# Kernel optimization log

Hardware: AMD Instinct MI355X
Metric: run time of the kernel (lower is better)

## Reference

```python
import jax, jax.numpy as jnp
import numpy as np

B, L, D = 16, 512, 128   # batch of sequences, seq len, input_dim
BN_EPS = 1e-5
TEMP = 1.0


def setup_inputs() -> dict:
    key = jax.random.key(0)
    ks = jax.random.split(key, 5)
    ids = jax.random.randint(ks[0], (B, L), 0, 50000)            # item ids per (seq, pos)
    log_mask = jnp.ones((B, L), dtype=jnp.int32)                 # all positions valid (static N)
    x1 = jax.random.normal(ks[1], (B * L, D), dtype=jnp.float32)
    x2 = jax.random.normal(ks[2], (B * L, D), dtype=jnp.float32)
    w1 = jax.random.normal(ks[3], (2 * D, D), dtype=jnp.float32) * 0.05  # torch Linear: [out, in]
    b1 = jnp.zeros((2 * D,), jnp.float32)
    w2 = jax.random.normal(ks[4], (D, 2 * D), dtype=jnp.float32) * 0.05
    b2 = jnp.zeros((D,), jnp.float32)
    gamma = jnp.ones((D,), jnp.float32)   # BatchNorm1d affine weight
    beta = jnp.zeros((D,), jnp.float32)   # BatchNorm1d affine bias
    return dict(ids=ids, log_mask=log_mask, x1=x1, x2=x2,
                w1=w1, b1=b1, w2=w2, b2=b2, gamma=gamma, beta=beta)


def _embed(x, w1, b1, w2, b2, gamma, beta):
    """linear1 -> relu -> linear2 -> BatchNorm1d (train-mode batch stats) -> L2 normalize."""
    h = jax.nn.relu(x @ w1.T + b1)
    y = h @ w2.T + b2
    mu = y.mean(axis=0)
    var = ((y - mu) ** 2).mean(axis=0)          # biased var, as torch BN uses for normalization
    y = (y - mu) * jax.lax.rsqrt(var + BN_EPS) * gamma + beta
    return y / jnp.linalg.norm(y, axis=1, keepdims=True)


def reference(ids, log_mask, x1, x2, w1, b1, w2, b2, gamma, beta):
    # log_mask is all-nonzero in this setup, so the gather by nonzero indices is the identity.
    nb, nl = ids.shape
    N = x1.shape[0]                      # = nb * nl valid anchors
    ids_f = ids.reshape(-1)
    seq = jnp.repeat(jnp.arange(nb), nl)  # seq_indexs: which sequence each row belongs to

    z1 = _embed(x1, w1, b1, w2, b2, gamma, beta)
    z2 = _embed(x2, w1, b1, w2, b2, gamma, beta)
    S = z1 @ z2.T                        # [N, N] cosine similarity (rows already unit-norm)

    idx = jnp.arange(N)
    ids_next = jnp.roll(ids_f, -1)
    seq_next = jnp.roll(seq, -1)
    # two-positive branch: i < N-1 and same sequence as the next row
    two = (idx < N - 1) & (seq == seq_next)            # [N] bool

    diag = jnp.diagonal(S)                             # cos(anchor_i, input2_i)
    s_next = S[idx, (idx + 1) % N]                     # cos(anchor_i, input2_{i+1})

    cols = idx[None, :]
    neg1 = ids_f[None, :] != ids_f[:, None]                                # single-pos negatives
    neg2 = neg1 & (ids_f[None, :] != ids_next[:, None]) & (seq[None, :] != seq[:, None])
    mask = jnp.where(two[:, None], neg2, neg1)
    # add the positives (self, and i+1 in the two-positive branch)
    mask = mask | (cols == idx[:, None]) | (two[:, None] & (cols == idx[:, None] + 1))

    denom = jnp.sum(jnp.where(mask, jnp.exp(S / TEMP), 0.0), axis=1)       # [N]
    pos_sum = diag + jnp.where(two, s_next, 0.0)
    n_pos = 1.0 + two.astype(S.dtype)

    inner = -(pos_sum / TEMP - jnp.log(denom)) / n_pos
    return jnp.sum(inner) / N
```

## Files before the change

### kernel.cpp

```cpp
#include <hip/hip_runtime.h>

#define N_TOT 8192
#define SEQ_L 512
#define D 128
#define NCHUNK 16
#define CHUNK (N_TOT / NCHUNK)
#define NJT (CHUNK / 64)
#define LOG2E 1.4426950408889634f
#define LN2   0.6931471805599453f

using bf16x8  = __attribute__((ext_vector_type(8))) short;
using f32x4   = __attribute__((ext_vector_type(4))) float;

static __device__ __forceinline__ unsigned short f2bf(float f) {
    unsigned int u = __float_as_uint(f);
    u = (u + 0x7FFFu + ((u >> 16) & 1u)) >> 16;
    return (unsigned short)u;
}
static __device__ __forceinline__ float bf2f(unsigned short h) {
    return __uint_as_float(((unsigned int)h) << 16);
}
static __device__ __forceinline__ float dot8(bf16x8 a, bf16x8 b) {
    float s = 0.f;
    #pragma unroll
    for (int k = 0; k < 8; ++k)
        s = fmaf(bf2f((unsigned short)a[k]), bf2f((unsigned short)b[k]), s);
    return s;
}

__global__ __launch_bounds__(256) void convert_w_kernel(
    const float* __restrict__ w1, const float* __restrict__ w2,
    unsigned short* __restrict__ w1b, unsigned short* __restrict__ w2b)
{
    int idx = blockIdx.x * 256 + threadIdx.x;
    const float* src = (idx < 8192) ? w1 : w2;
    unsigned short* dst = (idx < 8192) ? w1b : w2b;
    int off = ((idx < 8192) ? idx : idx - 8192) * 4;
    float4 v = *(const float4*)(src + off);
    ushort4 o;
    o.x = f2bf(v.x); o.y = f2bf(v.y); o.z = f2bf(v.z); o.w = f2bf(v.w);
    *(ushort4*)(dst + off) = o;
}

__global__ __launch_bounds__(256) void mlp_mfma_kernel(
    const float* __restrict__ x1, const float* __restrict__ x2,
    const unsigned short* __restrict__ w1b, const float* __restrict__ b1,
    const unsigned short* __restrict__ w2b, const float* __restrict__ b2,
    unsigned short* __restrict__ z1, unsigned short* __restrict__ z2,
    float* __restrict__ part_s, float* __restrict__ part_ss)
{
    __shared__ unsigned short hsh[32][264];
    const int t = threadIdx.x;
    const int w = t >> 6;
    const int lane = t & 63;
    const int g = lane >> 4;
    const int c16 = lane & 15;
    const int tensor = blockIdx.x >> 8;
    const int blk = blockIdx.x & 255;
    const int r0 = blk * 32;
    const float* __restrict__ x = tensor ? x2 : x1;
    unsigned short* __restrict__ z = tensor ? z2 : z1;

    bf16x8 af[2][4];
    #pragma unroll
    for (int rf = 0; rf < 2; ++rf)
        #pragma unroll
        for (int ks = 0; ks < 4; ++ks) {
            const float* xp = x + (size_t)(r0 + rf * 16 + c16) * D + ks * 32 + g * 8;
            float4 u0 = *(const float4*)xp;
            float4 u1 = *(const float4*)(xp + 4);
            bf16x8 a;
            a[0] = f2bf(u0.x); a[1] = f2bf(u0.y); a[2] = f2bf(u0.z); a[3] = f2bf(u0.w);
            a[4] = f2bf(u1.x); a[5] = f2bf(u1.y); a[6] = f2bf(u1.z); a[7] = f2bf(u1.w);
            af[rf][ks] = a;
        }
    f32x4 acc1[2][4] = {};
    #pragma unroll
    for (int ks = 0; ks < 4; ++ks)
        #pragma unroll
        for (int nf = 0; nf < 4; ++nf) {
            int n = w * 64 + nf * 16 + c16;
            bf16x8 b = *(const bf16x8*)(w1b + (size_t)n * D + ks * 32 + g * 8);
            #pragma unroll
            for (int rf = 0; rf < 2; ++rf)
                acc1[rf][nf] = __builtin_amdgcn_mfma_f32_16x16x32_bf16(af[rf][ks], b, acc1[rf][nf], 0, 0, 0);
        }
    #pragma unroll
    for (int nf = 0; nf < 4; ++nf) {
        float bb = b1[w * 64 + nf * 16 + c16];
        #pragma unroll
        for (int rf = 0; rf < 2; ++rf)
            #pragma unroll
            for (int r = 0; r < 4; ++r)
                hsh[rf * 16 + g * 4 + r][w * 64 + nf * 16 + c16] = f2bf(fmaxf(acc1[rf][nf][r] + bb, 0.f));
    }
    __syncthreads();

    f32x4 acc2[2][2] = {};
    #pragma unroll
    for (int ks = 0; ks < 8; ++ks) {
        bf16x8 a0 = *(const bf16x8*)(&hsh[c16][ks * 32 + g * 8]);
        bf16x8 a1 = *(const bf16x8*)(&hsh[16 + c16][ks * 32 + g * 8]);
        #pragma unroll
        for (int nf = 0; nf < 2; ++nf) {
            int n = w * 32 + nf * 16 + c16;
            bf16x8 b = *(const bf16x8*)(w2b + (size_t)n * 256 + ks * 32 + g * 8);
            acc2[0][nf] = __builtin_amdgcn_mfma_f32_16x16x32_bf16(a0, b, acc2[0][nf], 0, 0, 0);
            acc2[1][nf] = __builtin_amdgcn_mfma_f32_16x16x32_bf16(a1, b, acc2[1][nf], 0, 0, 0);
        }
    }

    #pragma unroll
    for (int nf = 0; nf < 2; ++nf) {
        int col = w * 32 + nf * 16 + c16;
        float bb = b2[col];
        float s = 0.f, ss = 0.f;
        #pragma unroll
        for (int rf = 0; rf < 2; ++rf)
            #pragma unroll
            for (int r = 0; r < 4; ++r) {
                float v = acc2[rf][nf][r] + bb;
                z[(size_t)(r0 + rf * 16 + g * 4 + r) * D + col] = f2bf(v);
                s += v; ss += v * v;
            }
        s  += __shfl_xor(s, 16);  s  += __shfl_xor(s, 32);
        ss += __shfl_xor(ss, 16); ss += __shfl_xor(ss, 32);
        if (g == 0) {
            part_s [((size_t)tensor * 256 + blk) * D + col] = s;
            part_ss[((size_t)tensor * 256 + blk) * D + col] = ss;
        }
    }
}

__global__ __launch_bounds__(256) void bn_reduce_kernel(
    const float* __restrict__ part_s, const float* __restrict__ part_ss,
    const float* __restrict__ gamma,
    float* __restrict__ mu, float* __restrict__ sc)
{
    const int t = threadIdx.x;
    const int tensor = blockIdx.x >> 7;
    const int col = blockIdx.x & 127;
    float s  = part_s [((size_t)tensor * 256 + t) * D + col];
    float ss = part_ss[((size_t)tensor * 256 + t) * D + col];
    #pragma unroll
    for (int m = 32; m; m >>= 1) { s += __shfl_xor(s, m); ss += __shfl_xor(ss, m); }
    __shared__ float rs[4], rss[4];
    if ((t & 63) == 0) { rs[t >> 6] = s; rss[t >> 6] = ss; }
    __syncthreads();
    if (t == 0) {
        float S = rs[0] + rs[1] + rs[2] + rs[3];
        float SS = rss[0] + rss[1] + rss[2] + rss[3];
        float m = S / (float)N_TOT;
        float var = SS / (float)N_TOT - m * m;
        mu[tensor * D + col] = m;
        sc[tensor * D + col] = gamma[col] * rsqrtf(var + 1e-5f);
    }
}

__global__ __launch_bounds__(256) void bn_l2_kernel(
    unsigned short* __restrict__ z1, unsigned short* __restrict__ z2,
    const float* __restrict__ mu, const float* __restrict__ sc,
    const float* __restrict__ beta)
{
    const int t = threadIdx.x;
    const int tensor = blockIdx.x >> 11;
    const int row = (blockIdx.x & 2047) * 4 + (t >> 6);
    const int lane = t & 63;
    unsigned short* __restrict__ yr = (tensor ? z2 : z1) + (size_t)row * D;
    const float* __restrict__ mub = mu + tensor * D;
    const float* __restrict__ scb = sc + tensor * D;

    ushort2 v = ((const ushort2*)yr)[lane];
    float2 m2 = ((const float2*)mub)[lane];
    float2 s2 = ((const float2*)scb)[lane];
    float2 b2 = ((const float2*)beta)[lane];
    float v0 = (bf2f(v.x) - m2.x) * s2.x + b2.x;
    float v1 = (bf2f(v.y) - m2.y) * s2.y + b2.y;
    float ssq = v0 * v0 + v1 * v1;
    #pragma unroll
    for (int m = 32; m; m >>= 1) ssq += __shfl_xor(ssq, m);
    float rn = rsqrtf(ssq);
    if (tensor == 0) rn *= LOG2E;
    ushort2 o; o.x = f2bf(v0 * rn); o.y = f2bf(v1 * rn);
    ((ushort2*)yr)[lane] = o;
}

__global__ __launch_bounds__(256) void diag_kernel(
    const short* __restrict__ z1, const short* __restrict__ z2,
    const int* __restrict__ ids,
    float* __restrict__ posv, float* __restrict__ dden)
{
    const int t = threadIdx.x;
    if (blockIdx.x < 256) {
        const int row = blockIdx.x * 32 + (t >> 3);
        const int le = t & 7;
        const short* ap = z1 + (size_t)row * D + le * 16;
        const short* bp = z2 + (size_t)row * D + le * 16;
        const short* cp = z2 + (size_t)((row + 1) & (N_TOT - 1)) * D + le * 16;
        bf16x8 a0 = *(const bf16x8*)ap, a1 = *(const bf16x8*)(ap + 8);
        float s1 = dot8(a0, *(const bf16x8*)bp) + dot8(a1, *(const bf16x8*)(bp + 8));
        float s2 = dot8(a0, *(const bf16x8*)cp) + dot8(a1, *(const bf16x8*)(cp + 8));
        #pragma unroll
        for (int m = 1; m < 8; m <<= 1) { s1 += __shfl_xor(s1, m); s2 += __shfl_xor(s2, m); }
        if (le == 0) {
            bool two = (row & (SEQ_L - 1)) != (SEQ_L - 1);
            if (two) {
                posv[row] = (s1 + s2) * LN2;
                dden[row] = exp2f(s1) + exp2f(s2);
            } else {
                posv[row] = s1 * LN2;
            }
        }
    } else {
        const int sr = blockIdx.x - 256;
        const int i = sr * SEQ_L + (SEQ_L - 1);
        const int jbase = sr * SEQ_L;
        const int idi_ = ids[i];
        float acc = 0.f;
        #pragma unroll
        for (int c = 0; c < 2; ++c) {
            int j = jbase + t * 2 + c;
            float s = 0.f;
            for (int k = 0; k < 16; ++k) {
                bf16x8 va = *(const bf16x8*)(z1 + (size_t)i * D + k * 8);
                bf16x8 vb = *(const bf16x8*)(z2 + (size_t)j * D + k * 8);
                s += dot8(va, vb);
            }
            bool m = (ids[j] != idi_) | (j == i);
            acc += m ? exp2f(s) : 0.f;
        }
        #pragma unroll
        for (int m = 32; m; m >>= 1) acc += __shfl_xor(acc, m);
        __shared__ float red[4];
        if ((t & 63) == 0) red[t >> 6] = acc;
        __syncthreads();
        if (t == 0) dden[i] = red[0] + red[1] + red[2] + red[3];
    }
}

__global__ __launch_bounds__(256) void loss_mfma_kernel(
    const short* __restrict__ z1, const short* __restrict__ z2,
    const int* __restrict__ ids,
    float* __restrict__ den_part)
{
    const int t    = threadIdx.x;
    const int w    = t >> 6;
    const int lane = t & 63;
    const int g    = lane >> 4;
    const int c16  = lane & 15;

    const int c15 = blockIdx.x >> 6;
    const int rbi = blockIdx.x & 63;
    const int rb  = rbi * 128;
    const int seqb = rbi >> 2;
    const int chunk = c15 + (c15 >= seqb);
    const int jbase = chunk * CHUNK;

    const int i_wb = rb + w * 32;

    __shared__ __align__(16) unsigned char z2s[2][64 * 256];

    const int srow = t >> 2;
    const int sq   = t & 3;

    bf16x8 af[2][4];
    #pragma unroll
    for (int rf = 0; rf < 2; ++rf)
        #pragma unroll
        for (int ks = 0; ks < 4; ++ks)
            af[rf][ks] = *(const bf16x8*)(z1 + (size_t)(i_wb + rf * 16 + c16) * D + ks * 32 + g * 8);

    int idi[2][4], idn_s[2][4];
    #pragma unroll
    for (int rf = 0; rf < 2; ++rf)
        #pragma unroll
        for (int r = 0; r < 4; ++r) {
            int i = i_wb + rf * 16 + g * 4 + r;
            idi[rf][r] = ids[i];
            bool tw = ((i & (SEQ_L - 1)) != (SEQ_L - 1));
            idn_s[rf][r] = tw ? ids[(i + 1) & (N_TOT - 1)] : idi[rf][r];
        }

    #pragma unroll
    for (int it = 0; it < 4; ++it) {
        bf16x8 v = *(const bf16x8*)(z2 + (size_t)(jbase + srow) * D + sq * 8 + it * 32);
        int byte = (sq * 16 + it * 64) ^ ((srow & 7) << 4);
        *(bf16x8*)&z2s[0][srow * 256 + byte] = v;
    }
    int idj[4];
    #pragma unroll
    for (int nf = 0; nf < 4; ++nf) idj[nf] = ids[jbase + nf * 16 + c16];
    __syncthreads();

    float den_acc[2][4] = {};
    int cbuf = 0;

    #pragma unroll 1
    for (int jt = 0; jt < NJT; ++jt) {
        const int cb = jbase + jt * 64;

        bf16x8 stg[4];
        int idjn[4];
        if (jt + 1 < NJT) {
            #pragma unroll
            for (int it = 0; it < 4; ++it)
                stg[it] = *(const bf16x8*)(z2 + (size_t)(cb + 64 + srow) * D + sq * 8 + it * 32);
            #pragma unroll
            for (int nf = 0; nf < 4; ++nf) idjn[nf] = ids[cb + 64 + nf * 16 + c16];
        }

        f32x4 acc[2][4] = {};
        #pragma unroll
        for (int ks = 0; ks < 4; ++ks)
            #pragma unroll
            for (int nf = 0; nf < 4; ++nf) {
                int r = nf * 16 + c16;
                int byte = (ks * 64 + g * 16) ^ ((r & 7) << 4);
                bf16x8 b = *(const bf16x8*)&z2s[cbuf][r * 256 + byte];
                acc[0][nf] = __builtin_amdgcn_mfma_f32_16x16x32_bf16(af[0][ks], b, acc[0][nf], 0, 0, 0);
                acc[1][nf] = __builtin_amdgcn_mfma_f32_16x16x32_bf16(af[1][ks], b, acc[1][nf], 0, 0, 0);
            }

        #pragma unroll
        for (int rf = 0; rf < 2; ++rf)
            #pragma unroll
            for (int nf = 0; nf < 4; ++nf)
                #pragma unroll
                for (int r = 0; r < 4; ++r) {
                    float e = exp2f(acc[rf][nf][r]);
                    bool m = (idj[nf] != idi[rf][r]) & (idj[nf] != idn_s[rf][r]);
                    den_acc[rf][r] += m ? e : 0.f;
                }

        if (jt + 1 < NJT) {
            #pragma unroll
            for (int it = 0; it < 4; ++it) {
                int byte = (sq * 16 + it * 64) ^ ((srow & 7) << 4);
                *(bf16x8*)&z2s[cbuf ^ 1][srow * 256 + byte] = stg[it];
            }
            #pragma unroll
            for (int nf = 0; nf < 4; ++nf) idj[nf] = idjn[nf];
        }
        __syncthreads();
        cbuf ^= 1;
    }

    #pragma unroll
    for (int rf = 0; rf < 2; ++rf)
        #pragma unroll
        for (int r = 0; r < 4; ++r) {
            float dsum = den_acc[rf][r];
            #pragma unroll
            for (int m = 8; m; m >>= 1) dsum += __shfl_xor(dsum, m);
            if (c16 == 0)
                den_part[chunk * N_TOT + i_wb + rf * 16 + g * 4 + r] = dsum;
        }
}

__global__ __launch_bounds__(1024) void loss_finish_kernel(
    const float* __restrict__ den_part, const float* __restrict__ posv,
    const float* __restrict__ dden, float* __restrict__ out)
{
    const int t = threadIdx.x;
    float v = 0.f;
    for (int k = 0; k < N_TOT / 1024; ++k) {
        int row = t + k * 1024;
        int seqb = row >> 9;
        float den = dden[row];
        #pragma unroll
        for (int q = 0; q < NCHUNK; ++q)
            if (q != seqb) den += den_part[q * N_TOT + row];
        bool two = ((row & (SEQ_L - 1)) != (SEQ_L - 1));
        float npos = two ? 2.f : 1.f;
        v += -(posv[row] - logf(den)) / npos;
    }
    #pragma unroll
    for (int m = 32; m; m >>= 1) v += __shfl_xor(v, m);
    __shared__ float red[16];
    if ((t & 63) == 0) red[t >> 6] = v;
    __syncthreads();
    if (t == 0) {
        float tot = 0.f;
        #pragma unroll
        for (int i = 0; i < 16; ++i) tot += red[i];
        out[0] = tot / (float)N_TOT;
    }
}

extern "C" void kernel_launch(void* const* d_in, const int* in_sizes, int n_in,
                              void* d_out, int out_size, void* d_ws, size_t ws_size,
                              hipStream_t stream)
{
    const int*   ids   = (const int*)d_in[0];
    const float* x1    = (const float*)d_in[2];
    const float* x2    = (const float*)d_in[3];
    const float* w1    = (const float*)d_in[4];
    const float* b1    = (const float*)d_in[5];
    const float* w2    = (const float*)d_in[6];
    const float* b2    = (const float*)d_in[7];
    const float* gamma = (const float*)d_in[8];
    const float* beta  = (const float*)d_in[9];

    char* ws = (char*)d_ws;
    unsigned short* z1b = (unsigned short*)ws;
    unsigned short* z2b = (unsigned short*)(ws + (2u << 20));
    float* part_s  = (float*)(ws + (4u << 20));
    float* part_ss = part_s + 2 * 256 * D;
    float* mu      = part_ss + 2 * 256 * D;
    float* sc      = mu + 2 * D;
    float* den_part = sc + 2 * D;
    float* posv    = den_part + NCHUNK * N_TOT;
    float* dden    = posv + N_TOT;
    unsigned short* w1b = (unsigned short*)(dden + N_TOT);
    unsigned short* w2b = w1b + 256 * D;

    convert_w_kernel<<<64, 256, 0, stream>>>(w1, w2, w1b, w2b);
    mlp_mfma_kernel<<<512, 256, 0, stream>>>(x1, x2, w1b, b1, w2b, b2,
                                             z1b, z2b, part_s, part_ss);
    bn_reduce_kernel<<<256, 256, 0, stream>>>(part_s, part_ss, gamma, mu, sc);
    bn_l2_kernel<<<4096, 256, 0, stream>>>(z1b, z2b, mu, sc, beta);
    diag_kernel<<<272, 256, 0, stream>>>((const short*)z1b, (const short*)z2b,
                                         ids, posv, dden);
    loss_mfma_kernel<<<960, 256, 0, stream>>>((const short*)z1b, (const short*)z2b,
                                              ids, den_part);
    loss_finish_kernel<<<1, 1024, 0, stream>>>(den_part, posv, dden, (float*)d_out);
}
```

Before: 89.45 us.

## Remove id masking from cross-sequence loss tile; subtract rare id collisions separately

The cross-sequence MFMA tile loop no longer loads ids or evaluates the negative mask per element. It sums exp over all columns, and a new corr_kernel computes the exp of the rare masked-out entries (id matches with the anchor or next id) so the finish kernel can subtract them. The loop is also restructured: the last tile is peeled, the LDS store and barrier move before the exp accumulation, and the kernel gets an occupancy hint in its launch bounds. The trade-off is an extra kernel that scans all ids for every row, plus possible cancellation error from subtracting large exp terms.

```diff
diff --git a/kernel.cpp b/kernel.cpp
--- a/kernel.cpp
+++ b/kernel.cpp
@@ -238,9 +238,58 @@
     }
 }
 
-__global__ __launch_bounds__(256) void loss_mfma_kernel(
+__global__ __launch_bounds__(256) void corr_kernel(
     const short* __restrict__ z1, const short* __restrict__ z2,
-    const int* __restrict__ ids,
+    const int* __restrict__ ids, float* __restrict__ corr)
+{
+    const int t = threadIdx.x;
+    const int w = t >> 6;
+    const int lane = t & 63;
+    const int rbase = blockIdx.x * 8 + w * 2;
+
+    int   idi[2], idn[2], seqi[2];
+    bool  two[2];
+    float cr[2] = {0.f, 0.f};
+    #pragma unroll
+    for (int rr = 0; rr < 2; ++rr) {
+        int i = rbase + rr;
+        idi[rr] = ids[i];
+        idn[rr] = ids[(i + 1) & (N_TOT - 1)];
+        two[rr] = (i & (SEQ_L - 1)) != (SEQ_L - 1);
+        seqi[rr] = i >> 9;
+    }
+
+    for (int k = 0; k < N_TOT / 64; ++k) {
+        int j = lane + k * 64;
+        int idj = ids[j];
+        int seqj = j >> 9;
+        #pragma unroll
+        for (int rr = 0; rr < 2; ++rr) {
+            bool hit = (seqj != seqi[rr]) &&
+                       ((idj == idi[rr]) || (two[rr] && idj == idn[rr]));
+            if (hit) {
+                int i = rbase + rr;
+                float s = 0.f;
+                for (int k2 = 0; k2 < 16; ++k2) {
+                    bf16x8 va = *(const bf16x8*)(z1 + (size_t)i * D + k2 * 8);
+                    bf16x8 vb = *(const bf16x8*)(z2 + (size_t)j * D + k2 * 8);
+                    s += dot8(va, vb);
+                }
+                cr[rr] += exp2f(s);
+            }
+        }
+    }
+    #pragma unroll
+    for (int rr = 0; rr < 2; ++rr) {
+        float v = cr[rr];
+        #pragma unroll
+        for (int m = 32; m; m >>= 1) v += __shfl_xor(v, m);
+        if (lane == 0) corr[rbase + rr] = v;
+    }
+}
+
+__global__ __launch_bounds__(256, 4) void loss_mfma_kernel(
+    const short* __restrict__ z1, const short* __restrict__ z2,
     float* __restrict__ den_part)
 {
     const int t    = threadIdx.x;
@@ -262,6 +311,8 @@
 
     const int srow = t >> 2;
     const int sq   = t & 3;
+    const int wxor = (srow & 7) << 4;
+    const int rxor = (c16 & 7) << 4;
 
     bf16x8 af[2][4];
     #pragma unroll
@@ -270,79 +321,67 @@
         for (int ks = 0; ks < 4; ++ks)
             af[rf][ks] = *(const bf16x8*)(z1 + (size_t)(i_wb + rf * 16 + c16) * D + ks * 32 + g * 8);
 
-    int idi[2][4], idn_s[2][4];
-    #pragma unroll
-    for (int rf = 0; rf < 2; ++rf)
-        #pragma unroll
-        for (int r = 0; r < 4; ++r) {
-            int i = i_wb + rf * 16 + g * 4 + r;
-            idi[rf][r] = ids[i];
-            bool tw = ((i & (SEQ_L - 1)) != (SEQ_L - 1));
-            idn_s[rf][r] = tw ? ids[(i + 1) & (N_TOT - 1)] : idi[rf][r];
-        }
-
     #pragma unroll
     for (int it = 0; it < 4; ++it) {
         bf16x8 v = *(const bf16x8*)(z2 + (size_t)(jbase + srow) * D + sq * 8 + it * 32);
-        int byte = (sq * 16 + it * 64) ^ ((srow & 7) << 4);
-        *(bf16x8*)&z2s[0][srow * 256 + byte] = v;
-    }
-    int idj[4];
-    #pragma unroll
-    for (int nf = 0; nf < 4; ++nf) idj[nf] = ids[jbase + nf * 16 + c16];
+        *(bf16x8*)&z2s[0][srow * 256 + ((sq * 16 + it * 64) ^ wxor)] = v;
+    }
     __syncthreads();
 
     float den_acc[2][4] = {};
     int cbuf = 0;
 
     #pragma unroll 1
-    for (int jt = 0; jt < NJT; ++jt) {
+    for (int jt = 0; jt < NJT - 1; ++jt) {
         const int cb = jbase + jt * 64;
 
         bf16x8 stg[4];
-        int idjn[4];
-        if (jt + 1 < NJT) {
-            #pragma unroll
-            for (int it = 0; it < 4; ++it)
-                stg[it] = *(const bf16x8*)(z2 + (size_t)(cb + 64 + srow) * D + sq * 8 + it * 32);
-            #pragma unroll
-            for (int nf = 0; nf < 4; ++nf) idjn[nf] = ids[cb + 64 + nf * 16 + c16];
-        }
+        #pragma unroll
+        for (int it = 0; it < 4; ++it)
+            stg[it] = *(const bf16x8*)(z2 + (size_t)(cb + 64 + srow) * D + sq * 8 + it * 32);
 
         f32x4 acc[2][4] = {};
         #pragma unroll
         for (int ks = 0; ks < 4; ++ks)
             #pragma unroll
             for (int nf = 0; nf < 4; ++nf) {
-                int r = nf * 16 + c16;
-                int byte = (ks * 64 + g * 16) ^ ((r & 7) << 4);
-                bf16x8 b = *(const bf16x8*)&z2s[cbuf][r * 256 + byte];
+                bf16x8 b = *(const bf16x8*)&z2s[cbuf][(nf * 16 + c16) * 256 + ((ks * 64 + g * 16) ^ rxor)];
                 acc[0][nf] = __builtin_amdgcn_mfma_f32_16x16x32_bf16(af[0][ks], b, acc[0][nf], 0, 0, 0);
                 acc[1][nf] = __builtin_amdgcn_mfma_f32_16x16x32_bf16(af[1][ks], b, acc[1][nf], 0, 0, 0);
             }
 
         #pragma unroll
+        for (int it = 0; it < 4; ++it)
+            *(bf16x8*)&z2s[cbuf ^ 1][srow * 256 + ((sq * 16 + it * 64) ^ wxor)] = stg[it];
+        __syncthreads();
+
+        #pragma unroll
         for (int rf = 0; rf < 2; ++rf)
             #pragma unroll
             for (int nf = 0; nf < 4; ++nf)
                 #pragma unroll
-                for (int r = 0; r < 4; ++r) {
-                    float e = exp2f(acc[rf][nf][r]);
-                    bool m = (idj[nf] != idi[rf][r]) & (idj[nf] != idn_s[rf][r]);
-                    den_acc[rf][r] += m ? e : 0.f;
-                }
-
-        if (jt + 1 < NJT) {
-            #pragma unroll
-            for (int it = 0; it < 4; ++it) {
-                int byte = (sq * 16 + it * 64) ^ ((srow & 7) << 4);
-                *(bf16x8*)&z2s[cbuf ^ 1][srow * 256 + byte] = stg[it];
-            }
-            #pragma unroll
-            for (int nf = 0; nf < 4; ++nf) idj[nf] = idjn[nf];
-        }
-        __syncthreads();
+                for (int r = 0; r < 4; ++r)
+                    den_acc[rf][r] += exp2f(acc[rf][nf][r]);
         cbuf ^= 1;
+    }
+
+    {
+        f32x4 acc[2][4] = {};
+        #pragma unroll
+        for (int ks = 0; ks < 4; ++ks)
+            #pragma unroll
+            for (int nf = 0; nf < 4; ++nf) {
+                bf16x8 b = *(const bf16x8*)&z2s[cbuf][(nf * 16 + c16) * 256 + ((ks * 64 + g * 16) ^ rxor)];
+                acc[0][nf] = __builtin_amdgcn_mfma_f32_16x16x32_bf16(af[0][ks], b, acc[0][nf], 0, 0, 0);
+                acc[1][nf] = __builtin_amdgcn_mfma_f32_16x16x32_bf16(af[1][ks], b, acc[1][nf], 0, 0, 0);
+            }
+        #pragma unroll
+        for (int rf = 0; rf < 2; ++rf)
+            #pragma unroll
+            for (int nf = 0; nf < 4; ++nf)
+                #pragma unroll
+                for (int r = 0; r < 4; ++r)
+                    den_acc[rf][r] += exp2f(acc[rf][nf][r]);
     }
 
     #pragma unroll
@@ -359,14 +398,15 @@
 
 __global__ __launch_bounds__(1024) void loss_finish_kernel(
     const float* __restrict__ den_part, const float* __restrict__ posv,
-    const float* __restrict__ dden, float* __restrict__ out)
+    const float* __restrict__ dden, const float* __restrict__ corr,
+    float* __restrict__ out)
 {
     const int t = threadIdx.x;
     float v = 0.f;
     for (int k = 0; k < N_TOT / 1024; ++k) {
         int row = t + k * 1024;
         int seqb = row >> 9;
-        float den = dden[row];
+        float den = dden[row] - corr[row];
         #pragma unroll
         for (int q = 0; q < NCHUNK; ++q)
             if (q != seqb) den += den_part[q * N_TOT + row];
@@ -411,7 +451,8 @@
     float* den_part = sc + 2 * D;
     float* posv    = den_part + NCHUNK * N_TOT;
     float* dden    = posv + N_TOT;
-    unsigned short* w1b = (unsigned short*)(dden + N_TOT);
+    float* corr    = dden + N_TOT;
+    unsigned short* w1b = (unsigned short*)(corr + N_TOT);
     unsigned short* w2b = w1b + 256 * D;
 
     convert_w_kernel<<<64, 256, 0, stream>>>(w1, w2, w1b, w2b);
@@ -421,7 +462,10 @@
     bn_l2_kernel<<<4096, 256, 0, stream>>>(z1b, z2b, mu, sc, beta);
     diag_kernel<<<272, 256, 0, stream>>>((const short*)z1b, (const short*)z2b,
                                          ids, posv, dden);
+    corr_kernel<<<1024, 256, 0, stream>>>((const short*)z1b, (const short*)z2b,
+                                          ids, corr);
     loss_mfma_kernel<<<960, 256, 0, stream>>>((const short*)z1b, (const short*)z2b,
-                                              ids, den_part);
-    loss_finish_kernel<<<1, 1024, 0, stream>>>(den_part, posv, dden, (float*)d_out);
-}
+                                              den_part);
+    loss_finish_kernel<<<1, 1024, 0, stream>>>(den_part, posv, dden, corr,
+                                               (float*)d_out);
+}
```

After: 114.9 us. 1.28x slower.

## Compute unmasked full-row exp sums and subtract sparse id-match corrections

Applied to the files above, without the earlier changes.

The dense loss kernel now sums exp(S) over every column without id masks. It computes all 16 chunks, including the own-sequence chunk, and drops the LDS staging in favour of direct per-wave global loads of z2 fragments. A new corr_kernel scans the ids per row and subtracts the exp terms of the rare columns whose id matches. The finish kernel swaps the own-sequence chunk for the diagonal term on two-positive rows. This removes per-element mask compares and the special-cased chunk skipping, at the cost of computing 1/16 more of the matrix, a serial per-row id scan, and loss of LDS reuse of z2 across waves.

```diff
diff --git a/kernel.cpp b/kernel.cpp
--- a/kernel.cpp
+++ b/kernel.cpp
@@ -5,7 +5,6 @@
 #define D 128
 #define NCHUNK 16
 #define CHUNK (N_TOT / NCHUNK)
-#define NJT (CHUNK / 64)
 #define LOG2E 1.4426950408889634f
 #define LN2   0.6931471805599453f
 
@@ -187,60 +186,79 @@
 
 __global__ __launch_bounds__(256) void diag_kernel(
     const short* __restrict__ z1, const short* __restrict__ z2,
-    const int* __restrict__ ids,
     float* __restrict__ posv, float* __restrict__ dden)
 {
     const int t = threadIdx.x;
-    if (blockIdx.x < 256) {
-        const int row = blockIdx.x * 32 + (t >> 3);
-        const int le = t & 7;
-        const short* ap = z1 + (size_t)row * D + le * 16;
-        const short* bp = z2 + (size_t)row * D + le * 16;
-        const short* cp = z2 + (size_t)((row + 1) & (N_TOT - 1)) * D + le * 16;
-        bf16x8 a0 = *(const bf16x8*)ap, a1 = *(const bf16x8*)(ap + 8);
-        float s1 = dot8(a0, *(const bf16x8*)bp) + dot8(a1, *(const bf16x8*)(bp + 8));
-        float s2 = dot8(a0, *(const bf16x8*)cp) + dot8(a1, *(const bf16x8*)(cp + 8));
-        #pragma unroll
-        for (int m = 1; m < 8; m <<= 1) { s1 += __shfl_xor(s1, m); s2 += __shfl_xor(s2, m); }
-        if (le == 0) {
-            bool two = (row & (SEQ_L - 1)) != (SEQ_L - 1);
-            if (two) {
-                posv[row] = (s1 + s2) * LN2;
-                dden[row] = exp2f(s1) + exp2f(s2);
-            } else {
-                posv[row] = s1 * LN2;
+    const int row = blockIdx.x * 32 + (t >> 3);
+    const int le = t & 7;
+    const short* ap = z1 + (size_t)row * D + le * 16;
+    const short* bp = z2 + (size_t)row * D + le * 16;
+    const short* cp = z2 + (size_t)((row + 1) & (N_TOT - 1)) * D + le * 16;
+    bf16x8 a0 = *(const bf16x8*)ap, a1 = *(const bf16x8*)(ap + 8);
+    float s1 = dot8(a0, *(const bf16x8*)bp) + dot8(a1, *(const bf16x8*)(bp + 8));
+    float s2 = dot8(a0, *(const bf16x8*)cp) + dot8(a1, *(const bf16x8*)(cp + 8));
+    #pragma unroll
+    for (int m = 1; m < 8; m <<= 1) { s1 += __shfl_xor(s1, m); s2 += __shfl_xor(s2, m); }
+    if (le == 0) {
+        bool two = (row & (SEQ_L - 1)) != (SEQ_L - 1);
+        if (two) {
+            posv[row] = (s1 + s2) * LN2;
+            dden[row] = exp2f(s1) + exp2f(s2);
+        } else {
+            posv[row] = s1 * LN2;
+        }
+    }
+}
+
+__global__ __launch_bounds__(256) void corr_kernel(
+    const short* __restrict__ z1, const short* __restrict__ z2,
+    const int* __restrict__ ids, float* __restrict__ corr)
+{
+    const int t = threadIdx.x;
+    const int row = blockIdx.x * 32 + (t >> 3);
+    const int le = t & 7;
+
+    const bool two = (row & (SEQ_L - 1)) != (SEQ_L - 1);
+    const int idi  = ids[row];
+    const int idn_s = two ? ids[(row + 1) & (N_TOT - 1)] : idi;
+    const int seq_s = two ? (row >> 9) : -1;
+
+    float cr = 0.f;
+    const int4* idv = (const int4*)ids;
+    #pragma unroll 4
+    for (int k = 0; k < 256; ++k) {
+        int jb = le * 256 + k;
+        int4 v = idv[jb];
+        int j0 = jb * 4;
+        if ((j0 >> 9) != seq_s) {
+            int hm = (((v.x == idi) | (v.x == idn_s)) & (j0 + 0 != row) ? 1 : 0)
+                   | (((v.y == idi) | (v.y == idn_s)) & (j0 + 1 != row) ? 2 : 0)
+                   | (((v.z == idi) | (v.z == idn_s)) & (j0 + 2 != row) ? 4 : 0)
+                   | (((v.w == idi) | (v.w == idn_s)) & (j0 + 3 != row) ? 8 : 0);
+            if (hm) {
+                #pragma unroll
+                for (int c = 0; c < 4; ++c)
+                    if (hm & (1 << c)) {
+                        int j = j0 + c;
+                        float s = 0.f;
+                        for (int k2 = 0; k2 < 16; ++k2) {
+                            bf16x8 va = *(const bf16x8*)(z1 + (size_t)row * D + k2 * 8);
+                            bf16x8 vb = *(const bf16x8*)(z2 + (size_t)j * D + k2 * 8);
+                            s += dot8(va, vb);
+                        }
+                        cr += exp2f(s);
+                    }
             }
         }
-    } else {
-        const int sr = blockIdx.x - 256;
-        const int i = sr * SEQ_L + (SEQ_L - 1);
-        const int jbase = sr * SEQ_L;
-        const int idi_ = ids[i];
-        float acc = 0.f;
-        #pragma unroll
-        for (int c = 0; c < 2; ++c) {
-            int j = jbase + t * 2 + c;
-            float s = 0.f;
-            for (int k = 0; k < 16; ++k) {
-                bf16x8 va = *(const bf16x8*)(z1 + (size_t)i * D + k * 8);
-                bf16x8 vb = *(const bf16x8*)(z2 + (size_t)j * D + k * 8);
-                s += dot8(va, vb);
-            }
-            bool m = (ids[j] != idi_) | (j == i);
-            acc += m ? exp2f(s) : 0.f;
-        }
-        #pragma unroll
-        for (int m = 32; m; m >>= 1) acc += __shfl_xor(acc, m);
-        __shared__ float red[4];
-        if ((t & 63) == 0) red[t >> 6] = acc;
-        __syncthreads();
-        if (t == 0) dden[i] = red[0] + red[1] + red[2] + red[3];
-    }
-}
-
-__global__ __launch_bounds__(256) void loss_mfma_kernel(
+    }
+    cr += __shfl_xor(cr, 1);
+    cr += __shfl_xor(cr, 2);
+    cr += __shfl_xor(cr, 4);
+    if (le == 0) corr[row] = cr;
+}
+
+__global__ __launch_bounds__(256) void loss_stream_kernel(
     const short* __restrict__ z1, const short* __restrict__ z2,
-    const int* __restrict__ ids,
     float* __restrict__ den_part)
 {
     const int t    = threadIdx.x;
@@ -249,128 +267,74 @@
     const int g    = lane >> 4;
     const int c16  = lane & 15;
 
-    const int c15 = blockIdx.x >> 6;
-    const int rbi = blockIdx.x & 63;
-    const int rb  = rbi * 128;
-    const int seqb = rbi >> 2;
-    const int chunk = c15 + (c15 >= seqb);
-    const int jbase = chunk * CHUNK;
-
-    const int i_wb = rb + w * 32;
-
-    __shared__ __align__(16) unsigned char z2s[2][64 * 256];
-
-    const int srow = t >> 2;
-    const int sq   = t & 3;
+    const int chunk = blockIdx.x & (NCHUNK - 1);
+    const int rb    = (blockIdx.x >> 4) * 32;
+    const int jw    = chunk * CHUNK + w * 128;
 
     bf16x8 af[2][4];
     #pragma unroll
     for (int rf = 0; rf < 2; ++rf)
         #pragma unroll
         for (int ks = 0; ks < 4; ++ks)
-            af[rf][ks] = *(const bf16x8*)(z1 + (size_t)(i_wb + rf * 16 + c16) * D + ks * 32 + g * 8);
-
-    int idi[2][4], idn_s[2][4];
+            af[rf][ks] = *(const bf16x8*)(z1 + (size_t)(rb + rf * 16 + c16) * D + ks * 32 + g * 8);
+
+    float den[2][4] = {};
+
+    #pragma unroll 1
+    for (int it = 0; it < 8; ++it) {
+        const int cb = jw + it * 16;
+        bf16x8 bfr[4];
+        #pragma unroll
+        for (int ks = 0; ks < 4; ++ks)
+            bfr[ks] = *(const bf16x8*)(z2 + (size_t)(cb + c16) * D + ks * 32 + g * 8);
+
+        f32x4 acc0 = {}, acc1 = {};
+        #pragma unroll
+        for (int ks = 0; ks < 4; ++ks) {
+            acc0 = __builtin_amdgcn_mfma_f32_16x16x32_bf16(af[0][ks], bfr[ks], acc0, 0, 0, 0);
+            acc1 = __builtin_amdgcn_mfma_f32_16x16x32_bf16(af[1][ks], bfr[ks], acc1, 0, 0, 0);
+        }
+        #pragma unroll
+        for (int r = 0; r < 4; ++r) {
+            den[0][r] += exp2f(acc0[r]);
+            den[1][r] += exp2f(acc1[r]);
+        }
+    }
+
+    __shared__ float sh_den[4][32];
     #pragma unroll
     for (int rf = 0; rf < 2; ++rf)
         #pragma unroll
         for (int r = 0; r < 4; ++r) {
-            int i = i_wb + rf * 16 + g * 4 + r;
-            idi[rf][r] = ids[i];
-            bool tw = ((i & (SEQ_L - 1)) != (SEQ_L - 1));
-            idn_s[rf][r] = tw ? ids[(i + 1) & (N_TOT - 1)] : idi[rf][r];
-        }
-
-    #pragma unroll
-    for (int it = 0; it < 4; ++it) {
-        bf16x8 v = *(const bf16x8*)(z2 + (size_t)(jbase + srow) * D + sq * 8 + it * 32);
-        int byte = (sq * 16 + it * 64) ^ ((srow & 7) << 4);
-        *(bf16x8*)&z2s[0][srow * 256 + byte] = v;
-    }
-    int idj[4];
-    #pragma unroll
-    for (int nf = 0; nf < 4; ++nf) idj[nf] = ids[jbase + nf * 16 + c16];
+            float d = den[rf][r];
+            d += __shfl_xor(d, 1);
+            d += __shfl_xor(d, 2);
+            d += __shfl_xor(d, 4);
+            d += __shfl_xor(d, 8);
+            if (c16 == 0) sh_den[w][rf * 16 + g * 4 + r] = d;
+        }
     __syncthreads();
-
-    float den_acc[2][4] = {};
-    int cbuf = 0;
-
-    #pragma unroll 1
-    for (int jt = 0; jt < NJT; ++jt) {
-        const int cb = jbase + jt * 64;
-
-        bf16x8 stg[4];
-        int idjn[4];
-        if (jt + 1 < NJT) {
-            #pragma unroll
-            for (int it = 0; it < 4; ++it)
-                stg[it] = *(const bf16x8*)(z2 + (size_t)(cb + 64 + srow) * D + sq * 8 + it * 32);
-            #pragma unroll
-            for (int nf = 0; nf < 4; ++nf) idjn[nf] = ids[cb + 64 + nf * 16 + c16];
-        }
-
-        f32x4 acc[2][4] = {};
-        #pragma unroll
-        for (int ks = 0; ks < 4; ++ks)
-            #pragma unroll
-            for (int nf = 0; nf < 4; ++nf) {
-                int r = nf * 16 + c16;
-                int byte = (ks * 64 + g * 16) ^ ((r & 7) << 4);
-                bf16x8 b = *(const bf16x8*)&z2s[cbuf][r * 256 + byte];
-                acc[0][nf] = __builtin_amdgcn_mfma_f32_16x16x32_bf16(af[0][ks], b, acc[0][nf], 0, 0, 0);
-                acc[1][nf] = __builtin_amdgcn_mfma_f32_16x16x32_bf16(af[1][ks], b, acc[1][nf], 0, 0, 0);
-            }
-
-        #pragma unroll
-        for (int rf = 0; rf < 2; ++rf)
-            #pragma unroll
-            for (int nf = 0; nf < 4; ++nf)
-                #pragma unroll
-                for (int r = 0; r < 4; ++r) {
-                    float e = exp2f(acc[rf][nf][r]);
-                    bool m = (idj[nf] != idi[rf][r]) & (idj[nf] != idn_s[rf][r]);
-                    den_acc[rf][r] += m ? e : 0.f;
-                }
-
-        if (jt + 1 < NJT) {
-            #pragma unroll
-            for (int it = 0; it < 4; ++it) {
-                int byte = (sq * 16 + it * 64) ^ ((srow & 7) << 4);
-                *(bf16x8*)&z2s[cbuf ^ 1][srow * 256 + byte] = stg[it];
-            }
-            #pragma unroll
-            for (int nf = 0; nf < 4; ++nf) idj[nf] = idjn[nf];
-        }
-        __syncthreads();
-        cbuf ^= 1;
-    }
-
-    #pragma unroll
-    for (int rf = 0; rf < 2; ++rf)
-        #pragma unroll
-        for (int r = 0; r < 4; ++r) {
-            float dsum = den_acc[rf][r];
-            #pragma unroll
-            for (int m = 8; m; m >>= 1) dsum += __shfl_xor(dsum, m);
-            if (c16 == 0)
-                den_part[chunk * N_TOT + i_wb + rf * 16 + g * 4 + r] = dsum;
-        }
+    if (t < 32)
+        den_part[chunk * N_TOT + rb + t] =
+            sh_den[0][t] + sh_den[1][t] + sh_den[2][t] + sh_den[3][t];
 }
 
 __global__ __launch_bounds__(1024) void loss_finish_kernel(
     const float* __restrict__ den_part, const float* __restrict__ posv,
-    const float* __restrict__ dden, float* __restrict__ out)
+    const float* __restrict__ dden, const float* __restrict__ corr,
+    float* __restrict__ out)
 {
     const int t = threadIdx.x;
     float v = 0.f;
     for (int k = 0; k < N_TOT / 1024; ++k) {
         int row = t + k * 1024;
         int seqb = row >> 9;
-        float den = dden[row];
-        #pragma unroll
-        for (int q = 0; q < NCHUNK; ++q)
-            if (q != seqb) den += den_part[q * N_TOT + row];
+        float s_all = 0.f;
+        #pragma unroll
+        for (int q = 0; q < NCHUNK; ++q) s_all += den_part[q * N_TOT + row];
         bool two = ((row & (SEQ_L - 1)) != (SEQ_L - 1));
+        float den = two ? (s_all - den_part[seqb * N_TOT + row] + dden[row] - corr[row])
+                        : (s_all - corr[row]);
         float npos = two ? 2.f : 1.f;
         v += -(posv[row] - logf(den)) / npos;
     }
@@ -411,7 +375,8 @@
     float* den_part = sc + 2 * D;
     float* posv    = den_part + NCHUNK * N_TOT;
     float* dden    = posv + N_TOT;
-    unsigned short* w1b = (unsigned short*)(dden + N_TOT);
+    float* corr    = dden + N_TOT;
+    unsigned short* w1b = (unsigned short*)(corr + N_TOT);
     unsigned short* w2b = w1b + 256 * D;
 
     convert_w_kernel<<<64, 256, 0, stream>>>(w1, w2, w1b, w2b);
@@ -419,9 +384,12 @@
                                              z1b, z2b, part_s, part_ss);
     bn_reduce_kernel<<<256, 256, 0, stream>>>(part_s, part_ss, gamma, mu, sc);
     bn_l2_kernel<<<4096, 256, 0, stream>>>(z1b, z2b, mu, sc, beta);
-    diag_kernel<<<272, 256, 0, stream>>>((const short*)z1b, (const short*)z2b,
-                                         ids, posv, dden);
-    loss_mfma_kernel<<<960, 256, 0, stream>>>((const short*)z1b, (const short*)z2b,
-                                              ids, den_part);
-    loss_finish_kernel<<<1, 1024, 0, stream>>>(den_part, posv, dden, (float*)d_out);
-}
+    diag_kernel<<<256, 256, 0, stream>>>((const short*)z1b, (const short*)z2b,
+                                         posv, dden);
+    corr_kernel<<<256, 256, 0, stream>>>((const short*)z1b, (const short*)z2b,
+                                         ids, corr);
+    loss_stream_kernel<<<4096, 256, 0, stream>>>((const short*)z1b, (const short*)z2b,
+                                                 den_part);
+    loss_finish_kernel<<<1, 1024, 0, stream>>>(den_part, posv, dden, corr,
+                                               (float*)d_out);
+}
```

New measurement: 184.7 us. 2.07x slower.

## Double rows per wave in loss kernel and move exp epilogue after the barrier

Applied to the files above, without the earlier changes.

Each wave now handles 64 anchor rows (4 MFMA row fragments) instead of 32, so each shared-memory B fragment feeds four MFMAs and the z2 tile is reused across twice as many rows. The grid halves to 480 blocks with a new block-to-chunk mapping. The next-tile LDS store and barrier now come before the exp/mask epilogue, which may let the epilogue overlap the other block's work. Register pressure rises (launch_bounds 256,2), and fewer blocks may leave some CUs underused.

```diff
diff --git a/kernel.cpp b/kernel.cpp
--- a/kernel.cpp
+++ b/kernel.cpp
@@ -238,7 +238,7 @@
     }
 }
 
-__global__ __launch_bounds__(256) void loss_mfma_kernel(
+__global__ __launch_bounds__(256, 2) void loss_mfma_kernel(
     const short* __restrict__ z1, const short* __restrict__ z2,
     const int* __restrict__ ids,
     float* __restrict__ den_part)
@@ -249,30 +249,32 @@
     const int g    = lane >> 4;
     const int c16  = lane & 15;
 
-    const int c15 = blockIdx.x >> 6;
-    const int rbi = blockIdx.x & 63;
-    const int rb  = rbi * 128;
-    const int seqb = rbi >> 2;
+    const int c15 = blockIdx.x % 15;
+    const int rbi = blockIdx.x / 15;
+    const int rb  = rbi * 256;
+    const int seqb = rb >> 9;
     const int chunk = c15 + (c15 >= seqb);
     const int jbase = chunk * CHUNK;
 
-    const int i_wb = rb + w * 32;
+    const int i_wb = rb + w * 64;
 
     __shared__ __align__(16) unsigned char z2s[2][64 * 256];
 
     const int srow = t >> 2;
     const int sq   = t & 3;
-
-    bf16x8 af[2][4];
-    #pragma unroll
-    for (int rf = 0; rf < 2; ++rf)
+    const int wxor = (srow & 7) << 4;
+    const int rxor = (c16 & 7) << 4;
+
+    bf16x8 af[4][4];
+    #pragma unroll
+    for (int rf = 0; rf < 4; ++rf)
         #pragma unroll
         for (int ks = 0; ks < 4; ++ks)
             af[rf][ks] = *(const bf16x8*)(z1 + (size_t)(i_wb + rf * 16 + c16) * D + ks * 32 + g * 8);
 
-    int idi[2][4], idn_s[2][4];
-    #pragma unroll
-    for (int rf = 0; rf < 2; ++rf)
+    int idi[4][4], idn_s[4][4];
+    #pragma unroll
+    for (int rf = 0; rf < 4; ++rf)
         #pragma unroll
         for (int r = 0; r < 4; ++r) {
             int i = i_wb + rf * 16 + g * 4 + r;
@@ -284,15 +286,11 @@
     #pragma unroll
     for (int it = 0; it < 4; ++it) {
         bf16x8 v = *(const bf16x8*)(z2 + (size_t)(jbase + srow) * D + sq * 8 + it * 32);
-        int byte = (sq * 16 + it * 64) ^ ((srow & 7) << 4);
-        *(bf16x8*)&z2s[0][srow * 256 + byte] = v;
-    }
-    int idj[4];
-    #pragma unroll
-    for (int nf = 0; nf < 4; ++nf) idj[nf] = ids[jbase + nf * 16 + c16];
+        *(bf16x8*)&z2s[0][srow * 256 + ((sq * 16 + it * 64) ^ wxor)] = v;
+    }
     __syncthreads();
 
-    float den_acc[2][4] = {};
+    float den[4][4] = {};
     int cbuf = 0;
 
     #pragma unroll 1
@@ -300,58 +298,56 @@
         const int cb = jbase + jt * 64;
 
         bf16x8 stg[4];
-        int idjn[4];
         if (jt + 1 < NJT) {
             #pragma unroll
             for (int it = 0; it < 4; ++it)
                 stg[it] = *(const bf16x8*)(z2 + (size_t)(cb + 64 + srow) * D + sq * 8 + it * 32);
-            #pragma unroll
-            for (int nf = 0; nf < 4; ++nf) idjn[nf] = ids[cb + 64 + nf * 16 + c16];
-        }
-
-        f32x4 acc[2][4] = {};
+        }
+
+        int idj[4];
+        #pragma unroll
+        for (int nf = 0; nf < 4; ++nf) idj[nf] = ids[cb + nf * 16 + c16];
+
+        f32x4 acc[4][4] = {};
         #pragma unroll
         for (int ks = 0; ks < 4; ++ks)
             #pragma unroll
             for (int nf = 0; nf < 4; ++nf) {
-                int r = nf * 16 + c16;
-                int byte = (ks * 64 + g * 16) ^ ((r & 7) << 4);
-                bf16x8 b = *(const bf16x8*)&z2s[cbuf][r * 256 + byte];
-                acc[0][nf] = __builtin_amdgcn_mfma_f32_16x16x32_bf16(af[0][ks], b, acc[0][nf], 0, 0, 0);
-                acc[1][nf] = __builtin_amdgcn_mfma_f32_16x16x32_bf16(af[1][ks], b, acc[1][nf], 0, 0, 0);
+                bf16x8 b = *(const bf16x8*)&z2s[cbuf][(nf * 16 + c16) * 256 + ((ks * 64 + g * 16) ^ rxor)];
+                #pragma unroll
+                for (int rf = 0; rf < 4; ++rf)
+                    acc[rf][nf] = __builtin_amdgcn_mfma_f32_16x16x32_bf16(af[rf][ks], b, acc[rf][nf], 0, 0, 0);
             }
 
-        #pragma unroll
-        for (int rf = 0; rf < 2; ++rf)
+        if (jt + 1 < NJT) {
+            #pragma unroll
+            for (int it = 0; it < 4; ++it)
+                *(bf16x8*)&z2s[cbuf ^ 1][srow * 256 + ((sq * 16 + it * 64) ^ wxor)] = stg[it];
+        }
+        __syncthreads();
+
+        #pragma unroll
+        for (int rf = 0; rf < 4; ++rf)
             #pragma unroll
             for (int nf = 0; nf < 4; ++nf)
                 #pragma unroll
                 for (int r = 0; r < 4; ++r) {
                     float e = exp2f(acc[rf][nf][r]);
                     bool m = (idj[nf] != idi[rf][r]) & (idj[nf] != idn_s[rf][r]);
-                    den_acc[rf][r] += m ? e : 0.f;
+                    den[rf][r] += m ? e : 0.f;
                 }
-
-        if (jt + 1 < NJT) {
-            #pragma unroll
-            for (int it = 0; it < 4; ++it) {
-                int byte = (sq * 16 + it * 64) ^ ((srow & 7) << 4);
-                *(bf16x8*)&z2s[cbuf ^ 1][srow * 256 + byte] = stg[it];
-            }
-            #pragma unroll
-            for (int nf = 0; nf < 4; ++nf) idj[nf] = idjn[nf];
-        }
-        __syncthreads();
         cbuf ^= 1;
     }
 
     #pragma unroll
-    for (int rf = 0; rf < 2; ++rf)
+    for (int rf = 0; rf < 4; ++rf)
         #pragma unroll
         for (int r = 0; r < 4; ++r) {
-            float dsum = den_acc[rf][r];
-            #pragma unroll
-            for (int m = 8; m; m >>= 1) dsum += __shfl_xor(dsum, m);
+            float dsum = den[rf][r];
+            dsum += __shfl_xor(dsum, 1);
+            dsum += __shfl_xor(dsum, 2);
+            dsum += __shfl_xor(dsum, 4);
+            dsum += __shfl_xor(dsum, 8);
             if (c16 == 0)
                 den_part[chunk * N_TOT + i_wb + rf * 16 + g * 4 + r] = dsum;
         }
@@ -421,7 +417,7 @@
     bn_l2_kernel<<<4096, 256, 0, stream>>>(z1b, z2b, mu, sc, beta);
     diag_kernel<<<272, 256, 0, stream>>>((const short*)z1b, (const short*)z2b,
                                          ids, posv, dden);
-    loss_mfma_kernel<<<960, 256, 0, stream>>>((const short*)z1b, (const short*)z2b,
+    loss_mfma_kernel<<<480, 256, 0, stream>>>((const short*)z1b, (const short*)z2b,
                                               ids, den_part);
     loss_finish_kernel<<<1, 1024, 0, stream>>>(den_part, posv, dden, (float*)d_out);
 }
```

Measured after the change: 87.02 us. 1.03x faster.
